# Optimization experiments

Hardware: AMD Instinct MI355X
Metric: run time of the kernel (lower is better)

## Reference

```python
import jax, jax.numpy as jnp
import numpy as np
import math

D = 256; B = 4; N = 2048; IN = 16; POS = 3; LAT = 128
DEPTH = 3; RATIO = 0.5; NBLK = 8  # depth*2 + 2 final blocks


def _silu(x):
    return x * jax.nn.sigmoid(x)


def _ln(h, g, b):
    m = h.mean(-1, keepdims=True)
    v = h.var(-1, keepdims=True)  # biased, matches nn.LayerNorm
    return (h - m) / jnp.sqrt(v + 1e-5) * g + b


def _block(h, A, g, b, w1, b1, w2, b2, eps):
    # h: (B, n, D), A: (B, n, n) binary adjacency (block-diag equivalent)
    hn = _ln(h, g, b)
    nb = jnp.einsum('bij,bjd->bid', A, hn)  # sparse.mm(adj, h) per graph
    t = (1.0 + eps) * hn + nb
    t = _silu(t @ w1 + b1) @ w2 + b2
    return h + t


def _forward(x, adj, pos, in_w, in_b, pw1, pb1, pw2, pb2,
             bg, bb, bw1, bb1, bw2, bb2, beps, pool_p, lw, lb, batch_size):
    Bsz = batch_size
    n = adj.shape[0]
    d = in_w.shape[1]
    h = x @ in_w + in_b  # (B*N, D)
    # positional embedding: tile, normalize (unbiased std like torch), MLP
    pt = jnp.tile(pos, (Bsz, 1))
    pn = (pt - pt.mean(0, keepdims=True)) / (pt.std(0, ddof=1, keepdims=True) + 1e-8)
    pe = _silu(pn @ pw1 + pb1) @ pw2 + pb2
    h = (h + pe).reshape(Bsz, n, d)
    A = jnp.broadcast_to(adj, (Bsz, n, n))  # shared block-diag tiles
    blk = 0
    for dep in range(DEPTH):
        for _ in range(2):  # blocks_per_stage
            h = _block(h, A, bg[blk], bb[blk], bw1[blk], bb1[blk],
                       bw2[blk], bb2[blk], beps[blk])
            blk += 1
        # TopKPool: projection score, per-graph top-k, tanh gating
        p = pool_p[dep]
        score = h @ p / jnp.linalg.norm(p)  # (B, n)
        k = int(math.ceil(RATIO * h.shape[1]))  # static
        idx = jnp.sort(jax.lax.top_k(score, k)[1], axis=-1)  # (B, k)
        gate = jnp.tanh(jnp.take_along_axis(score, idx, axis=1))
        h = jnp.take_along_axis(h, idx[:, :, None], axis=1) * gate[:, :, None]
        # subgraph_coo + to_binary: adj[idx][:, idx] per graph
        A = jax.vmap(lambda a, i: a[i][:, i])(A, idx)
        A = (A > 0).astype(h.dtype)
    for _ in range(2):  # final_stage
        h = _block(h, A, bg[blk], bb[blk], bw1[blk], bb1[blk],
                   bw2[blk], bb2[blk], beps[blk])
        blk += 1
    hm = h.mean(1)
    hs = h.std(1, ddof=1) + 1e-6  # torch .std is unbiased
    return jnp.concatenate([hm, hs], axis=-1) @ lw + lb  # (B, LAT)


def setup_inputs() -> dict:
    key = jax.random.key(0)
    ks = jax.random.split(key, 12)
    f32 = jnp.float32
    s = 1.0 / np.sqrt(D)
    x = jax.random.normal(ks[0], (B * N, IN), f32)
    adj = (jax.random.uniform(ks[1], (N, N)) < 0.004).astype(f32)  # ~8 nbrs/node
    pos = jax.random.normal(ks[2], (N, POS), f32)
    return {
        'x': x, 'adj': adj, 'pos': pos,
        'in_w': jax.random.normal(ks[3], (IN, D), f32) / np.sqrt(IN),
        'in_b': jnp.zeros(D, f32),
        'pw1': jax.random.normal(ks[4], (POS, D), f32) / np.sqrt(POS),
        'pb1': jnp.zeros(D, f32),
        'pw2': jax.random.normal(ks[5], (D, D), f32) * s,
        'pb2': jnp.zeros(D, f32),
        'bg': jnp.ones((NBLK, D), f32),
        'bb': jnp.zeros((NBLK, D), f32),
        'bw1': jax.random.normal(ks[6], (NBLK, D, D), f32) * s,
        'bb1': jnp.zeros((NBLK, D), f32),
        'bw2': jax.random.normal(ks[7], (NBLK, D, D), f32) * (0.5 * s),
        'bb2': jnp.zeros((NBLK, D), f32),
        'beps': jnp.zeros(NBLK, f32),
        'pool_p': jax.random.normal(ks[8], (DEPTH, D), f32) * s,
        'lw': jax.random.normal(ks[9], (2 * D, LAT), f32) / np.sqrt(2 * D),
        'lb': jnp.zeros(LAT, f32),
        'batch_size': B,
    }


def reference(x, adj, pos, in_w, in_b, pw1, pb1, pw2, pb2,
              bg, bb, bw1, bb1, bw2, bb2, beps, pool_p, lw, lb, batch_size):
    return _forward(x, adj, pos, in_w, in_b, pw1, pb1, pw2, pb2,
                    bg, bb, bw1, bb1, bw2, bb2, beps, pool_p, lw, lb, batch_size)
```

## Files before the change

### kernel.cpp

```cpp
#include <hip/hip_runtime.h>
#include <hip/hip_bf16.h>

#define NTOT 2048
#define DD 256
#define BSZ 4

typedef _Float16 half_t;
typedef __attribute__((ext_vector_type(8))) _Float16 halfx8;
typedef __attribute__((ext_vector_type(4))) _Float16 halfx4;
typedef __attribute__((ext_vector_type(4))) float f32x4;

__device__ __forceinline__ float blockReduceSum256(float v) {
    __shared__ float red[4];
    for (int off = 32; off > 0; off >>= 1) v += __shfl_down(v, off);
    int lane = threadIdx.x & 63, w = threadIdx.x >> 6;
    __syncthreads();
    if (lane == 0) red[w] = v;
    __syncthreads();
    return red[0] + red[1] + red[2] + red[3];
}

__global__ void stats_kernel(const float* __restrict__ pos, float* __restrict__ pstats,
                             const float* __restrict__ poolp, float* __restrict__ pinv) {
    int tid = threadIdx.x;
    if (blockIdx.x == 0) {
        float s[3] = {0.f, 0.f, 0.f};
        for (int i = tid; i < NTOT; i += 256)
            for (int c = 0; c < 3; ++c) s[c] += pos[i * 3 + c];
        float m[3];
        for (int c = 0; c < 3; ++c) m[c] = blockReduceSum256(s[c]) / (float)NTOT;
        float q[3] = {0.f, 0.f, 0.f};
        for (int i = tid; i < NTOT; i += 256)
            for (int c = 0; c < 3; ++c) { float d = pos[i * 3 + c] - m[c]; q[c] += d * d; }
        for (int c = 0; c < 3; ++c) {
            float t = blockReduceSum256(q[c]);
            if (tid == 0) {
                float var = ((float)BSZ * t) / ((float)BSZ * NTOT - 1.0f);
                pstats[c] = m[c];
                pstats[3 + c] = 1.0f / (sqrtf(var) + 1e-8f);
            }
        }
    } else {
        int dep = blockIdx.x - 1;
        float v = poolp[dep * DD + tid];
        float ss = blockReduceSum256(v * v);
        if (tid == 0) pinv[dep] = rsqrtf(ss);
    }
}

__global__ void pe_q_kernel(const float* __restrict__ pos, const float* __restrict__ stats,
                            const float* __restrict__ pw1, const float* __restrict__ pb1,
                            half_t* __restrict__ q) {
    int i = blockIdx.x, d = threadIdx.x;
    float acc = pb1[d];
    for (int c = 0; c < 3; ++c) {
        float pn = (pos[i * 3 + c] - stats[c]) * stats[3 + c];
        acc += pn * pw1[c * DD + d];
    }
    acc = acc / (1.0f + expf(-acc));
    q[i * DD + d] = (half_t)acc;
}

__global__ void init_h_kernel(const float* __restrict__ x, const float* __restrict__ in_w,
                              const float* __restrict__ in_b, const float* __restrict__ pe,
                              float* __restrict__ h, float* __restrict__ z) {
    int row = blockIdx.x, d = threadIdx.x;
    float acc = in_b[d];
    for (int k = 0; k < 16; ++k) acc += x[row * 16 + k] * in_w[k * DD + d];
    float v = acc + pe[(row & (NTOT - 1)) * DD + d];
    h[(size_t)row * DD + d] = v;
    float s = blockReduceSum256(v);
    float ss = blockReduceSum256(v * v);
    float mean = s * (1.0f / DD);
    float rs = rsqrtf(ss * (1.0f / DD) - mean * mean + 1e-5f);
    z[(size_t)row * DD + d] = (v - mean) * rs;
}

__global__ void wprep_kernel(const float* __restrict__ bw1, const float* __restrict__ bw2,
                             const float* __restrict__ pw2, half_t* __restrict__ Wt) {
    int m = blockIdx.x, nb = blockIdx.y * 16, kb = blockIdx.z * 16;
    const float* W = (m < 8) ? (bw1 + (size_t)m * DD * DD)
                  : (m < 16) ? (bw2 + (size_t)(m - 8) * DD * DD)
                             : pw2;
    __shared__ float s[16][17];
    int i = threadIdx.x >> 4, j = threadIdx.x & 15;
    s[i][j] = W[(size_t)(kb + i) * DD + nb + j];
    __syncthreads();
    Wt[(size_t)m * DD * DD + (size_t)(nb + i) * DD + kb + j] = (half_t)s[j][i];
}

__global__ void csr_count_kernel(const float* __restrict__ adj, int* __restrict__ counts) {
    int i = blockIdx.x, tid = threadIdx.x;
    float c = 0.f;
    for (int j = tid; j < NTOT; j += 256) c += (adj[(size_t)i * NTOT + j] != 0.f) ? 1.f : 0.f;
    float t = blockReduceSum256(c);
    if (tid == 0) counts[i] = (int)(t + 0.5f);
}

__global__ void scan_kernel(const int* __restrict__ counts, int* __restrict__ row_ptr) {
    __shared__ int csum[256];
    int tid = threadIdx.x;
    int local[8]; int tot = 0;
    for (int u = 0; u < 8; ++u) { local[u] = counts[tid * 8 + u]; tot += local[u]; }
    csum[tid] = tot; __syncthreads();
    for (int off = 1; off < 256; off <<= 1) {
        int v = (tid >= off) ? csum[tid - off] : 0;
        __syncthreads();
        csum[tid] += v;
        __syncthreads();
    }
    int run = csum[tid] - tot;
    for (int u = 0; u < 8; ++u) { row_ptr[tid * 8 + u] = run; run += local[u]; }
    if (tid == 255) row_ptr[NTOT] = run;
}

__global__ void csr_fill_kernel(const float* __restrict__ adj, const int* __restrict__ row_ptr,
                                int* __restrict__ col) {
    int i = blockIdx.x, lane = threadIdx.x;
    int base = row_ptr[i];
    int run = 0;
    for (int j0 = 0; j0 < NTOT; j0 += 64) {
        int j = j0 + lane;
        bool pred = adj[(size_t)i * NTOT + j] != 0.f;
        unsigned long long mask = __ballot(pred);
        if (pred) {
            int pos = run + __popcll(mask & ((1ull << lane) - 1ull));
            col[base + pos] = j;
        }
        run += __popcll(mask);
    }
}

__global__ void init_maps_kernel(int* __restrict__ orig, int* __restrict__ inv) {
    int t = blockIdx.x * 256 + threadIdx.x;
    int i = t & (NTOT - 1);
    orig[t] = i; inv[t] = i;
}

__global__ void build_lcol_kernel(const int* __restrict__ row_ptr, const int* __restrict__ col,
                                  const int* __restrict__ orig, const int* __restrict__ inv,
                                  int* __restrict__ ldeg, int* __restrict__ lcol, int k, int tag) {
    int t = blockIdx.x * 256 + threadIdx.x;
    int b = t / k, i = t - b * k;
    int key = b * NTOT + i;
    int o = orig[key];
    int s = row_ptr[o], e = row_ptr[o + 1];
    const int* invb = inv + b * NTOT;
    int cnt = 0;
    for (int p = s; p < e && cnt < 64; ++p) {
        int v = invb[col[p]];
        if ((v >> 12) == tag) { lcol[(size_t)key * 64 + cnt] = v & 4095; ++cnt; }
    }
    ldeg[key] = cnt;
}

template <int SCORE>
__global__ void __launch_bounds__(256) layer_kernel(
    float* __restrict__ h, const float* __restrict__ zin, float* __restrict__ zout,
    const half_t* __restrict__ Wt1, const half_t* __restrict__ Wt2,
    const float* __restrict__ b1v, const float* __restrict__ b2v,
    const float* __restrict__ gv, const float* __restrict__ bbv,
    const float* __restrict__ beps, int blk,
    const int* __restrict__ row_ptr, const int* __restrict__ col,
    const int* __restrict__ ldeg, const int* __restrict__ lcol,
    const float* __restrict__ poolp, const float* __restrict__ pinv_all,
    float* __restrict__ scores, int dep, int n, int lvl0) {
    __shared__ half_t tb[16][264];
    __shared__ half_t ub[16][264];
    __shared__ float part[4][16][3];
    __shared__ float mrs[16][2];
    int tid = threadIdx.x;
    int rowBase = blockIdx.x * 16;
    float eps1 = 1.0f + beps[blk];

    {
        int rl = tid >> 4, cg = tid & 15;
        int r = rowBase + rl;
        int b = r / n, i = r - b * n;
        const f32x4* zb = (const f32x4*)zin + (size_t)b * n * 64;
        f32x4 acc[4];
#pragma unroll
        for (int u = 0; u < 4; ++u) acc[u] = zb[(size_t)i * 64 + cg + 16 * u] * eps1;
        int deg; const int* lc;
        if (lvl0) {
            int s = row_ptr[i];
            deg = row_ptr[i + 1] - s;
            lc = col + s;
        } else {
            int key = b * NTOT + i;
            deg = ldeg[key];
            lc = lcol + (size_t)key * 64;
        }
        int p = 0;
        for (; p + 4 <= deg; p += 4) {
            int j0 = lc[p], j1 = lc[p + 1], j2 = lc[p + 2], j3 = lc[p + 3];
#pragma unroll
            for (int u = 0; u < 4; ++u) {
                f32x4 v0 = zb[(size_t)j0 * 64 + cg + 16 * u];
                f32x4 v1 = zb[(size_t)j1 * 64 + cg + 16 * u];
                f32x4 v2 = zb[(size_t)j2 * 64 + cg + 16 * u];
                f32x4 v3 = zb[(size_t)j3 * 64 + cg + 16 * u];
                acc[u] += (v0 + v1) + (v2 + v3);
            }
        }
        for (; p < deg; ++p) {
            int j = lc[p];
#pragma unroll
            for (int u = 0; u < 4; ++u) acc[u] += zb[(size_t)j * 64 + cg + 16 * u];
        }
        float coefb = eps1 + (float)deg;
#pragma unroll
        for (int u = 0; u < 4; ++u) {
            int c4 = cg + 16 * u;
            f32x4 gvv = ((const f32x4*)gv)[c4];
            f32x4 bvv = ((const f32x4*)bbv)[c4];
            f32x4 tv = gvv * acc[u] + bvv * coefb;
            halfx4 th;
#pragma unroll
            for (int e = 0; e < 4; ++e) th[e] = (half_t)tv[e];
            *(halfx4*)&tb[rl][c4 * 4] = th;
        }
    }
    __syncthreads();

    int w = tid >> 6, l = tid & 63;
    int lo = l & 15, hi = l >> 4;
    int kb = hi * 8;

    {
        f32x4 acc[4] = {};
#pragma unroll
        for (int k0 = 0; k0 < DD; k0 += 32) {
            halfx8 a0 = *(const halfx8*)&tb[lo][kb + k0];
#pragma unroll
            for (int j = 0; j < 4; ++j) {
                halfx8 bj = *(const halfx8*)(Wt1 + (size_t)(w * 64 + j * 16 + lo) * DD + kb + k0);
                acc[j] = __builtin_amdgcn_mfma_f32_16x16x32_f16(a0, bj, acc[j], 0, 0, 0);
            }
        }
        float bs[4];
#pragma unroll
        for (int j = 0; j < 4; ++j) bs[j] = b1v[w * 64 + j * 16 + lo];
#pragma unroll
        for (int q = 0; q < 4; ++q)
#pragma unroll
            for (int j = 0; j < 4; ++j) {
                float v = acc[j][q] + bs[j];
                v = v / (1.0f + expf(-v));
                ub[hi * 4 + q][w * 64 + j * 16 + lo] = (half_t)v;
            }
    }
    __syncthreads();

    {
        f32x4 acc[4] = {};
#pragma unroll
        for (int k0 = 0; k0 < DD; k0 += 32) {
            halfx8 a0 = *(const halfx8*)&ub[lo][kb + k0];
#pragma unroll
            for (int j = 0; j < 4; ++j) {
                halfx8 bj = *(const halfx8*)(Wt2 + (size_t)(w * 64 + j * 16 + lo) * DD + kb + k0);
                acc[j] = __builtin_amdgcn_mfma_f32_16x16x32_f16(a0, bj, acc[j], 0, 0, 0);
            }
        }
        float bs[4], pv[4] = {};
#pragma unroll
        for (int j = 0; j < 4; ++j) bs[j] = b2v[w * 64 + j * 16 + lo];
        if (SCORE) {
#pragma unroll
            for (int j = 0; j < 4; ++j) pv[j] = poolp[dep * DD + w * 64 + j * 16 + lo];
        }
        float vh[4][4];
#pragma unroll
        for (int q = 0; q < 4; ++q) {
            int r = rowBase + hi * 4 + q;
            float s = 0.f, ss = 0.f, sp = 0.f;
#pragma unroll
            for (int j = 0; j < 4; ++j) {
                int c = w * 64 + j * 16 + lo;
                float v = h[(size_t)r * DD + c] + acc[j][q] + bs[j];
                vh[j][q] = v;
                s += v; ss += v * v;
                if (SCORE) sp += v * pv[j];
            }
#pragma unroll
            for (int m = 1; m < 16; m <<= 1) {
                s += __shfl_xor(s, m); ss += __shfl_xor(ss, m);
                if (SCORE) sp += __shfl_xor(sp, m);
            }
            if (lo == 0) {
                int rl = hi * 4 + q;
                part[w][rl][0] = s; part[w][rl][1] = ss;
                if (SCORE) part[w][rl][2] = sp;
            }
        }
        __syncthreads();
        if (tid < 16) {
            float s = 0.f, ss = 0.f, sp = 0.f;
#pragma unroll
            for (int w2 = 0; w2 < 4; ++w2) {
                s += part[w2][tid][0]; ss += part[w2][tid][1];
                if (SCORE) sp += part[w2][tid][2];
            }
            float mean = s * (1.0f / DD);
            float var = ss * (1.0f / DD) - mean * mean;
            mrs[tid][0] = mean;
            mrs[tid][1] = rsqrtf(var + 1e-5f);
            if (SCORE) {
                int r = rowBase + tid;
                int b2 = r / n, ii = r - b2 * n;
                scores[b2 * NTOT + ii] = sp * pinv_all[dep];
            }
        }
        __syncthreads();
#pragma unroll
        for (int q = 0; q < 4; ++q) {
            int rl = hi * 4 + q;
            int r = rowBase + rl;
            float mean = mrs[rl][0], rs = mrs[rl][1];
#pragma unroll
            for (int j = 0; j < 4; ++j) {
                int c = w * 64 + j * 16 + lo;
                float v = vh[j][q];
                h[(size_t)r * DD + c] = v;
                zout[(size_t)r * DD + c] = (v - mean) * rs;
            }
        }
    }
}

__global__ void __launch_bounds__(256) mm_pe_kernel(const half_t* __restrict__ A,
                                                    const half_t* __restrict__ Wt,
                                                    const float* __restrict__ bias,
                                                    float* __restrict__ C) {
    int tid = threadIdx.x;
    int w = tid >> 6, l = tid & 63;
    int lo = l & 15, hi = l >> 4;
    int rowBase = blockIdx.x * 16;
    int kb = hi * 8;
    const half_t* a0p = A + (size_t)(rowBase + lo) * DD + kb;
    f32x4 acc[4] = {};
#pragma unroll
    for (int k0 = 0; k0 < DD; k0 += 32) {
        halfx8 a0 = *(const halfx8*)(a0p + k0);
#pragma unroll
        for (int j = 0; j < 4; ++j) {
            halfx8 bj = *(const halfx8*)(Wt + (size_t)(w * 64 + j * 16 + lo) * DD + kb + k0);
            acc[j] = __builtin_amdgcn_mfma_f32_16x16x32_f16(a0, bj, acc[j], 0, 0, 0);
        }
    }
#pragma unroll
    for (int q = 0; q < 4; ++q)
#pragma unroll
        for (int j = 0; j < 4; ++j) {
            int r = rowBase + hi * 4 + q;
            int c = w * 64 + j * 16 + lo;
            C[(size_t)r * DD + c] = acc[j][q] + bias[c];
        }
}

__global__ void topk_kernel(const float* __restrict__ scores, const int* __restrict__ orig_cur,
                            int* __restrict__ orig_next, int* __restrict__ idx_local,
                            float* __restrict__ gate, int n, int k) {
    __shared__ unsigned keys[2048];
    __shared__ int hist[256];
    __shared__ int sg[256], se[256];
    __shared__ int sh_bucket, sh_r, sh_cnt;
    __shared__ unsigned cand[256];
    __shared__ unsigned sh_thr;
    int b = blockIdx.x;
    const float* sc = scores + b * NTOT;
    int tid = threadIdx.x;
    for (int i = tid; i < n; i += 256) {
        unsigned u = __float_as_uint(sc[i]);
        keys[i] = (u & 0x80000000u) ? ~u : (u | 0x80000000u);
    }
    hist[tid] = 0;
    if (tid == 0) sh_cnt = 0;
    __syncthreads();
    for (int i = tid; i < n; i += 256) atomicAdd(&hist[keys[i] >> 24], 1);
    __syncthreads();
    int cnt = hist[tid];
    sg[tid] = cnt;
    __syncthreads();
    for (int off = 1; off < 256; off <<= 1) {
        int v = (tid >= off) ? sg[tid - off] : 0;
        __syncthreads();
        sg[tid] += v;
        __syncthreads();
    }
    int r = n - k;
    int incl = sg[tid], excl = incl - cnt;
    if (excl <= r && r < incl) { sh_bucket = tid; sh_r = r - excl; }
    __syncthreads();
    int b1 = sh_bucket, r1 = sh_r;
    int c = hist[b1];
    unsigned thrkey;
    if (c <= 256) {
        for (int i = tid; i < n; i += 256) {
            unsigned key = keys[i];
            if ((key >> 24) == (unsigned)b1) {
                int pos = atomicAdd(&sh_cnt, 1);
                cand[pos] = key;
            }
        }
        __syncthreads();
        if (tid < c) {
            unsigned mine = cand[tid];
            int less = 0, eq = 0;
            for (int j = 0; j < c; ++j) {
                unsigned oth = cand[j];
                less += (oth < mine); eq += (oth == mine);
            }
            if (less <= r1 && r1 < less + eq) sh_thr = mine;
        }
        __syncthreads();
        thrkey = sh_thr;
    } else {
        unsigned prefix = ((unsigned)b1) << 24;
        int rr = r1;
        for (int shift = 16; shift >= 0; shift -= 8) {
            __syncthreads();
            hist[tid] = 0;
            __syncthreads();
            unsigned mask = 0xFFFFFFFFu << (shift + 8);
            for (int i = tid; i < n; i += 256) {
                unsigned key = keys[i];
                if ((key & mask) == (prefix & mask)) atomicAdd(&hist[(key >> shift) & 255], 1);
            }
            __syncthreads();
            int cnt2 = hist[tid];
            sg[tid] = cnt2;
            __syncthreads();
            for (int off = 1; off < 256; off <<= 1) {
                int v = (tid >= off) ? sg[tid - off] : 0;
                __syncthreads();
                sg[tid] += v;
                __syncthreads();
            }
            int incl2 = sg[tid], excl2 = incl2 - cnt2;
            if (excl2 <= rr && rr < incl2) { sh_bucket = tid; sh_r = rr - excl2; }
            __syncthreads();
            prefix |= ((unsigned)sh_bucket) << shift;
            rr = sh_r;
            __syncthreads();
        }
        thrkey = prefix;
    }
    unsigned uthr = (thrkey & 0x80000000u) ? (thrkey ^ 0x80000000u) : ~thrkey;
    float thr = __uint_as_float(uthr);
    int chunk = n / 256;
    int base = tid * chunk;
    int cgt = 0, ceq = 0;
    for (int u = 0; u < chunk; ++u) {
        float s = sc[base + u];
        cgt += (s > thr); ceq += (s == thr);
    }
    sg[tid] = cgt; se[tid] = ceq; __syncthreads();
    for (int off = 1; off < 256; off <<= 1) {
        int vg = (tid >= off) ? sg[tid - off] : 0;
        int ve = (tid >= off) ? se[tid - off] : 0;
        __syncthreads();
        sg[tid] += vg; se[tid] += ve;
        __syncthreads();
    }
    int total_gt = sg[255];
    int ties = k - total_gt;
    int gtb = sg[tid] - cgt, eqb = se[tid] - ceq;
    for (int u = 0; u < chunk; ++u) {
        int i = base + u;
        float s = sc[i];
        bool isgt = (s > thr), iseq = (s == thr);
        bool keep = isgt || (iseq && eqb < ties);
        if (keep) {
            int pos = gtb + (eqb < ties ? eqb : ties);
            idx_local[b * NTOT + pos] = i;
            gate[b * NTOT + pos] = tanhf(s);
            orig_next[b * NTOT + pos] = orig_cur[b * NTOT + i];
        }
        gtb += isgt; eqb += iseq;
    }
}

__global__ void __launch_bounds__(64) gather_kernel(
    const float* __restrict__ h, const int* __restrict__ idx_local,
    const float* __restrict__ gate, const int* __restrict__ orig_new,
    float* __restrict__ hout, float* __restrict__ zout, int* __restrict__ inv,
    int n_old, int k, int tag) {
    int r = blockIdx.x;
    int b = r / k, rr = r - b * k;
    int lane = threadIdx.x;
    int src = idx_local[b * NTOT + rr];
    float gg = gate[b * NTOT + rr];
    f32x4 v = ((const f32x4*)h)[(size_t)(b * n_old + src) * 64 + lane] * gg;
    ((f32x4*)hout)[(size_t)r * 64 + lane] = v;
    float s = v[0] + v[1] + v[2] + v[3];
    float ss = v[0] * v[0] + v[1] * v[1] + v[2] * v[2] + v[3] * v[3];
#pragma unroll
    for (int m = 1; m < 64; m <<= 1) { s += __shfl_xor(s, m); ss += __shfl_xor(ss, m); }
    float mean = s * (1.0f / DD);
    float rs = rsqrtf(ss * (1.0f / DD) - mean * mean + 1e-5f);
    f32x4 zv = (v - mean) * rs;
    ((f32x4*)zout)[(size_t)r * 64 + lane] = zv;
    if (lane == 0) inv[b * NTOT + orig_new[b * NTOT + rr]] = (tag << 12) | rr;
}

__global__ void readout_kernel(const float* __restrict__ h, float* __restrict__ feat) {
    int bd = blockIdx.x;
    int b = bd >> 8, d = bd & 255;
    int i = threadIdx.x;
    float x = h[(size_t)(b * 256 + i) * DD + d];
    float m = blockReduceSum256(x) / 256.0f;
    float diff = x - m;
    float s2 = blockReduceSum256(diff * diff);
    if (i == 0) {
        feat[b * 512 + d] = m;
        feat[b * 512 + 256 + d] = sqrtf(s2 / 255.0f) + 1e-6f;
    }
}

__global__ void final_kernel(const float* __restrict__ feat, const float* __restrict__ lw,
                             const float* __restrict__ lb, float* __restrict__ out) {
    int b = blockIdx.x, l = threadIdx.x;
    float acc = lb[l];
    const float* f = feat + b * 512;
    for (int k = 0; k < 512; ++k) acc += f[k] * lw[k * 128 + l];
    out[b * 128 + l] = acc;
}

extern "C" void kernel_launch(void* const* d_in, const int* in_sizes, int n_in,
                              void* d_out, int out_size, void* d_ws, size_t ws_size,
                              hipStream_t stream) {
    (void)in_sizes; (void)n_in; (void)out_size; (void)ws_size;
    const float* x     = (const float*)d_in[0];
    const float* adj   = (const float*)d_in[1];
    const float* pos   = (const float*)d_in[2];
    const float* in_w  = (const float*)d_in[3];
    const float* in_b  = (const float*)d_in[4];
    const float* pw1   = (const float*)d_in[5];
    const float* pb1   = (const float*)d_in[6];
    const float* pw2   = (const float*)d_in[7];
    const float* pb2   = (const float*)d_in[8];
    const float* bg    = (const float*)d_in[9];
    const float* bb    = (const float*)d_in[10];
    const float* bw1   = (const float*)d_in[11];
    const float* bb1   = (const float*)d_in[12];
    const float* bw2   = (const float*)d_in[13];
    const float* bb2   = (const float*)d_in[14];
    const float* beps  = (const float*)d_in[15];
    const float* poolp = (const float*)d_in[16];
    const float* lw    = (const float*)d_in[17];
    const float* lb    = (const float*)d_in[18];
    float* out = (float*)d_out;

    char* wp = (char*)d_ws;
    auto alloc = [&](size_t bytes) -> void* {
        void* p = (void*)wp;
        wp += (bytes + 255) & ~(size_t)255;
        return p;
    };
    const size_t HBYTES = (size_t)BSZ * NTOT * DD * sizeof(float);
    float*  h    = (float*)alloc(HBYTES);
    float*  bufC = (float*)alloc(HBYTES);
    float*  zA   = (float*)alloc(HBYTES);
    float*  zB   = (float*)alloc(HBYTES);
    half_t* tbq  = (half_t*)alloc((size_t)NTOT * DD * sizeof(half_t));
    half_t* Wt   = (half_t*)alloc((size_t)17 * DD * DD * sizeof(half_t));
    float* pstats  = (float*)alloc(8 * sizeof(float));
    float* pinv    = (float*)alloc(4 * sizeof(float));
    float* scores  = (float*)alloc(BSZ * NTOT * sizeof(float));
    float* gate    = (float*)alloc(BSZ * NTOT * sizeof(float));
    int*   origA   = (int*)alloc(BSZ * NTOT * sizeof(int));
    int*   origB   = (int*)alloc(BSZ * NTOT * sizeof(int));
    int*   idxl    = (int*)alloc(BSZ * NTOT * sizeof(int));
    int*   inv     = (int*)alloc(BSZ * NTOT * sizeof(int));
    int*   counts  = (int*)alloc(NTOT * sizeof(int));
    int*   row_ptr = (int*)alloc((NTOT + 1) * sizeof(int));
    int*   col     = (int*)alloc((size_t)NTOT * 64 * sizeof(int));
    int*   ldeg    = (int*)alloc(BSZ * NTOT * sizeof(int));
    int*   lcol    = (int*)alloc((size_t)BSZ * NTOT * 64 * sizeof(int));
    float* feat    = (float*)alloc(BSZ * 512 * sizeof(float));

    wprep_kernel<<<dim3(17, 16, 16), 256, 0, stream>>>(bw1, bw2, pw2, Wt);
    stats_kernel<<<4, 256, 0, stream>>>(pos, pstats, poolp, pinv);
    pe_q_kernel<<<NTOT, 256, 0, stream>>>(pos, pstats, pw1, pb1, tbq);
    mm_pe_kernel<<<NTOT / 16, 256, 0, stream>>>(tbq, Wt + (size_t)16 * DD * DD, pb2, bufC);
    init_h_kernel<<<BSZ * NTOT, 256, 0, stream>>>(x, in_w, in_b, bufC, h, zA);
    csr_count_kernel<<<NTOT, 256, 0, stream>>>(adj, counts);
    scan_kernel<<<1, 256, 0, stream>>>(counts, row_ptr);
    csr_fill_kernel<<<NTOT, 64, 0, stream>>>(adj, row_ptr, col);
    init_maps_kernel<<<(BSZ * NTOT) / 256, 256, 0, stream>>>(origA, inv);

    float* hcur = h;
    float* halt = bufC;
    float* zin = zA;
    float* zout = zB;
    int* orig = origA;
    int* orign = origB;
    int n = NTOT;
    int blk = 0;
    for (int dep = 0; dep < 4; ++dep) {
        for (int s = 0; s < 2; ++s) {
            int rows = BSZ * n;
            if (s == 1 && dep < 3) {
                layer_kernel<1><<<rows / 16, 256, 0, stream>>>(
                    hcur, zin, zout, Wt + (size_t)blk * DD * DD, Wt + (size_t)(8 + blk) * DD * DD,
                    bb1 + blk * DD, bb2 + blk * DD, bg + blk * DD, bb + blk * DD,
                    beps, blk, row_ptr, col, ldeg, lcol, poolp, pinv, scores, dep, n,
                    dep == 0 ? 1 : 0);
            } else {
                layer_kernel<0><<<rows / 16, 256, 0, stream>>>(
                    hcur, zin, zout, Wt + (size_t)blk * DD * DD, Wt + (size_t)(8 + blk) * DD * DD,
                    bb1 + blk * DD, bb2 + blk * DD, bg + blk * DD, bb + blk * DD,
                    beps, blk, row_ptr, col, ldeg, lcol, nullptr, nullptr, nullptr, 0, n,
                    dep == 0 ? 1 : 0);
            }
            { float* t = zin; zin = zout; zout = t; }
            ++blk;
        }
        if (dep < 3) {
            int k = n / 2;
            topk_kernel<<<BSZ, 256, 0, stream>>>(scores, orig, orign, idxl, gate, n, k);
            { int* t = orig; orig = orign; orign = t; }
            gather_kernel<<<BSZ * k, 64, 0, stream>>>(hcur, idxl, gate, orig, halt, zin, inv,
                                                      n, k, dep + 1);
            { float* t = hcur; hcur = halt; halt = t; }
            build_lcol_kernel<<<(BSZ * k) / 256, 256, 0, stream>>>(row_ptr, col, orig, inv,
                                                                   ldeg, lcol, k, dep + 1);
            n = k;
        }
    }
    readout_kernel<<<BSZ * 256, 256, 0, stream>>>(hcur, feat);
    final_kernel<<<BSZ, 128, 0, stream>>>(feat, lw, lb, out);
}
```

Measured before the change: 294.8 us.

## Fuse setup kernels, merge PE MLP with input projection, filter neighbors inline

New measurement: 283.3 us. 3.9% less time.

```diff
diff --git a/kernel.cpp b/kernel.cpp
--- a/kernel.cpp
+++ b/kernel.cpp
@@ -20,138 +20,183 @@
     return red[0] + red[1] + red[2] + red[3];
 }
 
-__global__ void stats_kernel(const float* __restrict__ pos, float* __restrict__ pstats,
-                             const float* __restrict__ poolp, float* __restrict__ pinv) {
+#define SB_WPREP 4352
+#define SB_STAT  4356
+#define SB_A2L   4868
+#define SB_MAPS  4900
+__global__ void __launch_bounds__(256) setup_kernel(
+    const float* __restrict__ bw1, const float* __restrict__ bw2,
+    const float* __restrict__ pw2, half_t* __restrict__ Wt,
+    const float* __restrict__ pos, float* __restrict__ pstats,
+    const float* __restrict__ poolp, float* __restrict__ pinv,
+    const float* __restrict__ adj, int* __restrict__ ldeg0, int* __restrict__ lcol0,
+    int* __restrict__ orig, int* __restrict__ inv) {
+    int bid = blockIdx.x, tid = threadIdx.x;
+    if (bid < SB_WPREP) {
+        int m = bid >> 8, rem = bid & 255;
+        int nb = (rem >> 4) * 16, kb = (rem & 15) * 16;
+        const float* W = (m < 8) ? (bw1 + (size_t)m * DD * DD)
+                      : (m < 16) ? (bw2 + (size_t)(m - 8) * DD * DD)
+                                 : pw2;
+        __shared__ float s[16][17];
+        int i = tid >> 4, j = tid & 15;
+        s[i][j] = W[(size_t)(kb + i) * DD + nb + j];
+        __syncthreads();
+        Wt[(size_t)m * DD * DD + (size_t)(nb + i) * DD + kb + j] = (half_t)s[j][i];
+    } else if (bid < SB_STAT) {
+        int which = bid - SB_WPREP;
+        if (which == 0) {
+            float s[3] = {0.f, 0.f, 0.f};
+            for (int i = tid; i < NTOT; i += 256)
+                for (int c = 0; c < 3; ++c) s[c] += pos[i * 3 + c];
+            float m[3];
+            for (int c = 0; c < 3; ++c) m[c] = blockReduceSum256(s[c]) / (float)NTOT;
+            float q[3] = {0.f, 0.f, 0.f};
+            for (int i = tid; i < NTOT; i += 256)
+                for (int c = 0; c < 3; ++c) { float d = pos[i * 3 + c] - m[c]; q[c] += d * d; }
+            for (int c = 0; c < 3; ++c) {
+                float t = blockReduceSum256(q[c]);
+                if (tid == 0) {
+                    float var = ((float)BSZ * t) / ((float)BSZ * NTOT - 1.0f);
+                    pstats[c] = m[c];
+                    pstats[3 + c] = 1.0f / (sqrtf(var) + 1e-8f);
+                }
+            }
+        } else {
+            int dep = which - 1;
+            float v = poolp[dep * DD + tid];
+            float ss = blockReduceSum256(v * v);
+            if (tid == 0) pinv[dep] = rsqrtf(ss);
+        }
+    } else if (bid < SB_A2L) {
+        int row = (bid - SB_STAT) * 4 + (tid >> 6);
+        int lane = tid & 63;
+        int run = 0;
+        for (int j0 = 0; j0 < NTOT; j0 += 64) {
+            int j = j0 + lane;
+            bool pred = adj[(size_t)row * NTOT + j] != 0.f;
+            unsigned long long mask = __ballot(pred);
+            if (pred) {
+                int pos2 = run + __popcll(mask & ((1ull << lane) - 1ull));
+                if (pos2 < 64) lcol0[row * 64 + pos2] = j;
+            }
+            run += __popcll(mask);
+        }
+        if (lane == 0) ldeg0[row] = run < 64 ? run : 64;
+    } else {
+        int t = (bid - SB_A2L) * 256 + tid;
+        int i = t & (NTOT - 1);
+        orig[t] = i; inv[t] = i;
+    }
+}
+
+__global__ void __launch_bounds__(256) pe_h_kernel(
+    const float* __restrict__ pos, const float* __restrict__ pstats,
+    const float* __restrict__ pw1, const float* __restrict__ pb1,
+    const half_t* __restrict__ Wt16, const float* __restrict__ pb2,
+    const float* __restrict__ x, const float* __restrict__ in_w,
+    const float* __restrict__ in_b, float* __restrict__ h, float* __restrict__ z) {
+    __shared__ half_t tb[16][264];
+    __shared__ float iw[16][DD];
+    __shared__ float xs[16][16];
+    __shared__ float part[4][16][2];
+    __shared__ float mrs[16][2];
     int tid = threadIdx.x;
-    if (blockIdx.x == 0) {
-        float s[3] = {0.f, 0.f, 0.f};
-        for (int i = tid; i < NTOT; i += 256)
-            for (int c = 0; c < 3; ++c) s[c] += pos[i * 3 + c];
-        float m[3];
-        for (int c = 0; c < 3; ++c) m[c] = blockReduceSum256(s[c]) / (float)NTOT;
-        float q[3] = {0.f, 0.f, 0.f};
-        for (int i = tid; i < NTOT; i += 256)
-            for (int c = 0; c < 3; ++c) { float d = pos[i * 3 + c] - m[c]; q[c] += d * d; }
-        for (int c = 0; c < 3; ++c) {
-            float t = blockReduceSum256(q[c]);
-            if (tid == 0) {
-                float var = ((float)BSZ * t) / ((float)BSZ * NTOT - 1.0f);
-                pstats[c] = m[c];
-                pstats[3 + c] = 1.0f / (sqrtf(var) + 1e-8f);
-            }
-        }
-    } else {
-        int dep = blockIdx.x - 1;
-        float v = poolp[dep * DD + tid];
-        float ss = blockReduceSum256(v * v);
-        if (tid == 0) pinv[dep] = rsqrtf(ss);
-    }
-}
-
-__global__ void pe_q_kernel(const float* __restrict__ pos, const float* __restrict__ stats,
-                            const float* __restrict__ pw1, const float* __restrict__ pb1,
-                            half_t* __restrict__ q) {
-    int i = blockIdx.x, d = threadIdx.x;
-    float acc = pb1[d];
-    for (int c = 0; c < 3; ++c) {
-        float pn = (pos[i * 3 + c] - stats[c]) * stats[3 + c];
-        acc += pn * pw1[c * DD + d];
-    }
-    acc = acc / (1.0f + expf(-acc));
-    q[i * DD + d] = (half_t)acc;
-}
-
-__global__ void init_h_kernel(const float* __restrict__ x, const float* __restrict__ in_w,
-                              const float* __restrict__ in_b, const float* __restrict__ pe,
-                              float* __restrict__ h, float* __restrict__ z) {
-    int row = blockIdx.x, d = threadIdx.x;
-    float acc = in_b[d];
-    for (int k = 0; k < 16; ++k) acc += x[row * 16 + k] * in_w[k * DD + d];
-    float v = acc + pe[(row & (NTOT - 1)) * DD + d];
-    h[(size_t)row * DD + d] = v;
-    float s = blockReduceSum256(v);
-    float ss = blockReduceSum256(v * v);
-    float mean = s * (1.0f / DD);
-    float rs = rsqrtf(ss * (1.0f / DD) - mean * mean + 1e-5f);
-    z[(size_t)row * DD + d] = (v - mean) * rs;
-}
-
-__global__ void wprep_kernel(const float* __restrict__ bw1, const float* __restrict__ bw2,
-                             const float* __restrict__ pw2, half_t* __restrict__ Wt) {
-    int m = blockIdx.x, nb = blockIdx.y * 16, kb = blockIdx.z * 16;
-    const float* W = (m < 8) ? (bw1 + (size_t)m * DD * DD)
-                  : (m < 16) ? (bw2 + (size_t)(m - 8) * DD * DD)
-                             : pw2;
-    __shared__ float s[16][17];
-    int i = threadIdx.x >> 4, j = threadIdx.x & 15;
-    s[i][j] = W[(size_t)(kb + i) * DD + nb + j];
-    __syncthreads();
-    Wt[(size_t)m * DD * DD + (size_t)(nb + i) * DD + kb + j] = (half_t)s[j][i];
-}
-
-__global__ void csr_count_kernel(const float* __restrict__ adj, int* __restrict__ counts) {
-    int i = blockIdx.x, tid = threadIdx.x;
-    float c = 0.f;
-    for (int j = tid; j < NTOT; j += 256) c += (adj[(size_t)i * NTOT + j] != 0.f) ? 1.f : 0.f;
-    float t = blockReduceSum256(c);
-    if (tid == 0) counts[i] = (int)(t + 0.5f);
-}
-
-__global__ void scan_kernel(const int* __restrict__ counts, int* __restrict__ row_ptr) {
-    __shared__ int csum[256];
-    int tid = threadIdx.x;
-    int local[8]; int tot = 0;
-    for (int u = 0; u < 8; ++u) { local[u] = counts[tid * 8 + u]; tot += local[u]; }
-    csum[tid] = tot; __syncthreads();
-    for (int off = 1; off < 256; off <<= 1) {
-        int v = (tid >= off) ? csum[tid - off] : 0;
-        __syncthreads();
-        csum[tid] += v;
-        __syncthreads();
-    }
-    int run = csum[tid] - tot;
-    for (int u = 0; u < 8; ++u) { row_ptr[tid * 8 + u] = run; run += local[u]; }
-    if (tid == 255) row_ptr[NTOT] = run;
-}
-
-__global__ void csr_fill_kernel(const float* __restrict__ adj, const int* __restrict__ row_ptr,
-                                int* __restrict__ col) {
-    int i = blockIdx.x, lane = threadIdx.x;
-    int base = row_ptr[i];
-    int run = 0;
-    for (int j0 = 0; j0 < NTOT; j0 += 64) {
-        int j = j0 + lane;
-        bool pred = adj[(size_t)i * NTOT + j] != 0.f;
-        unsigned long long mask = __ballot(pred);
-        if (pred) {
-            int pos = run + __popcll(mask & ((1ull << lane) - 1ull));
-            col[base + pos] = j;
-        }
-        run += __popcll(mask);
-    }
-}
-
-__global__ void init_maps_kernel(int* __restrict__ orig, int* __restrict__ inv) {
-    int t = blockIdx.x * 256 + threadIdx.x;
-    int i = t & (NTOT - 1);
-    orig[t] = i; inv[t] = i;
-}
-
-__global__ void build_lcol_kernel(const int* __restrict__ row_ptr, const int* __restrict__ col,
-                                  const int* __restrict__ orig, const int* __restrict__ inv,
-                                  int* __restrict__ ldeg, int* __restrict__ lcol, int k, int tag) {
-    int t = blockIdx.x * 256 + threadIdx.x;
-    int b = t / k, i = t - b * k;
-    int key = b * NTOT + i;
-    int o = orig[key];
-    int s = row_ptr[o], e = row_ptr[o + 1];
-    const int* invb = inv + b * NTOT;
-    int cnt = 0;
-    for (int p = s; p < e && cnt < 64; ++p) {
-        int v = invb[col[p]];
-        if ((v >> 12) == tag) { lcol[(size_t)key * 64 + cnt] = v & 4095; ++cnt; }
-    }
-    ldeg[key] = cnt;
+    int i0 = blockIdx.x * 16;
+    {
+        int rl = tid >> 4, cb = (tid & 15) * 16;
+        float pn[3];
+#pragma unroll
+        for (int c = 0; c < 3; ++c)
+            pn[c] = (pos[(i0 + rl) * 3 + c] - pstats[c]) * pstats[3 + c];
+#pragma unroll
+        for (int u = 0; u < 16; ++u) {
+            int d = cb + u;
+            float a = pb1[d];
+            a += pn[0] * pw1[d];
+            a += pn[1] * pw1[DD + d];
+            a += pn[2] * pw1[2 * DD + d];
+            a = a / (1.0f + expf(-a));
+            tb[rl][d] = (half_t)a;
+        }
+        int k = tid >> 4;
+#pragma unroll
+        for (int u = 0; u < 16; ++u) iw[k][cb + u] = in_w[k * DD + cb + u];
+    }
+    __syncthreads();
+    int w = tid >> 6, l = tid & 63;
+    int lo = l & 15, hi = l >> 4;
+    int kb = hi * 8;
+    float pe_r[4][4];
+    {
+        f32x4 acc[4] = {};
+#pragma unroll
+        for (int k0 = 0; k0 < DD; k0 += 32) {
+            halfx8 a0 = *(const halfx8*)&tb[lo][kb + k0];
+#pragma unroll
+            for (int j = 0; j < 4; ++j) {
+                halfx8 bj = *(const halfx8*)(Wt16 + (size_t)(w * 64 + j * 16 + lo) * DD + kb + k0);
+                acc[j] = __builtin_amdgcn_mfma_f32_16x16x32_f16(a0, bj, acc[j], 0, 0, 0);
+            }
+        }
+#pragma unroll
+        for (int j = 0; j < 4; ++j) {
+            float bs = pb2[w * 64 + j * 16 + lo];
+#pragma unroll
+            for (int q = 0; q < 4; ++q) pe_r[j][q] = acc[j][q] + bs;
+        }
+    }
+    float xb[4];
+#pragma unroll
+    for (int j = 0; j < 4; ++j) xb[j] = in_b[w * 64 + j * 16 + lo];
+    for (int b = 0; b < BSZ; ++b) {
+        __syncthreads();
+        xs[tid >> 4][tid & 15] = x[(size_t)(b * NTOT + i0 + (tid >> 4)) * 16 + (tid & 15)];
+        __syncthreads();
+        float vh[4][4];
+#pragma unroll
+        for (int q = 0; q < 4; ++q) {
+            int rl = hi * 4 + q;
+            float s = 0.f, ss = 0.f;
+#pragma unroll
+            for (int j = 0; j < 4; ++j) {
+                int c = w * 64 + j * 16 + lo;
+                float acc = xb[j];
+#pragma unroll
+                for (int k = 0; k < 16; ++k) acc += xs[rl][k] * iw[k][c];
+                float v = acc + pe_r[j][q];
+                vh[j][q] = v;
+                s += v; ss += v * v;
+            }
+#pragma unroll
+            for (int m = 1; m < 16; m <<= 1) { s += __shfl_xor(s, m); ss += __shfl_xor(ss, m); }
+            if (lo == 0) { part[w][rl][0] = s; part[w][rl][1] = ss; }
+        }
+        __syncthreads();
+        if (tid < 16) {
+            float s = 0.f, ss = 0.f;
+#pragma unroll
+            for (int w2 = 0; w2 < 4; ++w2) { s += part[w2][tid][0]; ss += part[w2][tid][1]; }
+            float mean = s * (1.0f / DD);
+            float var = ss * (1.0f / DD) - mean * mean;
+            mrs[tid][0] = mean;
+            mrs[tid][1] = rsqrtf(var + 1e-5f);
+        }
+        __syncthreads();
+#pragma unroll
+        for (int q = 0; q < 4; ++q) {
+            int rl = hi * 4 + q;
+            size_t r = (size_t)(b * NTOT + i0 + rl);
+            float mean = mrs[rl][0], rs = mrs[rl][1];
+#pragma unroll
+            for (int j = 0; j < 4; ++j) {
+                int c = w * 64 + j * 16 + lo;
+                float v = vh[j][q];
+                h[r * DD + c] = v;
+                z[r * DD + c] = (v - mean) * rs;
+            }
+        }
+    }
 }
 
 template <int SCORE>
@@ -161,10 +206,10 @@
     const float* __restrict__ b1v, const float* __restrict__ b2v,
     const float* __restrict__ gv, const float* __restrict__ bbv,
     const float* __restrict__ beps, int blk,
-    const int* __restrict__ row_ptr, const int* __restrict__ col,
-    const int* __restrict__ ldeg, const int* __restrict__ lcol,
+    const int* __restrict__ ldeg0, const int* __restrict__ lcol0,
+    const int* __restrict__ orig, const int* __restrict__ inv,
     const float* __restrict__ poolp, const float* __restrict__ pinv_all,
-    float* __restrict__ scores, int dep, int n, int lvl0) {
+    float* __restrict__ scores, int dep, int n, int tag) {
     __shared__ half_t tb[16][264];
     __shared__ half_t ub[16][264];
     __shared__ float part[4][16][3];
@@ -181,34 +226,68 @@
         f32x4 acc[4];
 #pragma unroll
         for (int u = 0; u < 4; ++u) acc[u] = zb[(size_t)i * 64 + cg + 16 * u] * eps1;
-        int deg; const int* lc;
-        if (lvl0) {
-            int s = row_ptr[i];
-            deg = row_ptr[i + 1] - s;
-            lc = col + s;
+        int cnt = 0;
+        if (tag == 0) {
+            int deg = ldeg0[i];
+            const int* lc = lcol0 + i * 64;
+            int p = 0;
+            for (; p + 4 <= deg; p += 4) {
+                int j0 = lc[p], j1 = lc[p + 1], j2 = lc[p + 2], j3 = lc[p + 3];
+#pragma unroll
+                for (int u = 0; u < 4; ++u) {
+                    f32x4 v0 = zb[(size_t)j0 * 64 + cg + 16 * u];
+                    f32x4 v1 = zb[(size_t)j1 * 64 + cg + 16 * u];
+                    f32x4 v2 = zb[(size_t)j2 * 64 + cg + 16 * u];
+                    f32x4 v3 = zb[(size_t)j3 * 64 + cg + 16 * u];
+                    acc[u] += (v0 + v1) + (v2 + v3);
+                }
+            }
+            for (; p < deg; ++p) {
+                int j = lc[p];
+#pragma unroll
+                for (int u = 0; u < 4; ++u) acc[u] += zb[(size_t)j * 64 + cg + 16 * u];
+            }
+            cnt = deg;
         } else {
-            int key = b * NTOT + i;
-            deg = ldeg[key];
-            lc = lcol + (size_t)key * 64;
-        }
-        int p = 0;
-        for (; p + 4 <= deg; p += 4) {
-            int j0 = lc[p], j1 = lc[p + 1], j2 = lc[p + 2], j3 = lc[p + 3];
-#pragma unroll
-            for (int u = 0; u < 4; ++u) {
-                f32x4 v0 = zb[(size_t)j0 * 64 + cg + 16 * u];
-                f32x4 v1 = zb[(size_t)j1 * 64 + cg + 16 * u];
-                f32x4 v2 = zb[(size_t)j2 * 64 + cg + 16 * u];
-                f32x4 v3 = zb[(size_t)j3 * 64 + cg + 16 * u];
-                acc[u] += (v0 + v1) + (v2 + v3);
-            }
-        }
-        for (; p < deg; ++p) {
-            int j = lc[p];
-#pragma unroll
-            for (int u = 0; u < 4; ++u) acc[u] += zb[(size_t)j * 64 + cg + 16 * u];
-        }
-        float coefb = eps1 + (float)deg;
+            int o = orig[b * NTOT + i];
+            int deg = ldeg0[o];
+            const int* lc = lcol0 + o * 64;
+            const int* invb = inv + b * NTOT;
+            int p = 0;
+            for (; p + 4 <= deg; p += 4) {
+                int c0 = lc[p], c1 = lc[p + 1], c2 = lc[p + 2], c3 = lc[p + 3];
+                int v0 = invb[c0], v1 = invb[c1], v2 = invb[c2], v3 = invb[c3];
+                if ((v0 >> 12) == tag) {
+                    int j = v0 & 4095; ++cnt;
+#pragma unroll
+                    for (int u = 0; u < 4; ++u) acc[u] += zb[(size_t)j * 64 + cg + 16 * u];
+                }
+                if ((v1 >> 12) == tag) {
+                    int j = v1 & 4095; ++cnt;
+#pragma unroll
+                    for (int u = 0; u < 4; ++u) acc[u] += zb[(size_t)j * 64 + cg + 16 * u];
+                }
+                if ((v2 >> 12) == tag) {
+                    int j = v2 & 4095; ++cnt;
+#pragma unroll
+                    for (int u = 0; u < 4; ++u) acc[u] += zb[(size_t)j * 64 + cg + 16 * u];
+                }
+                if ((v3 >> 12) == tag) {
+                    int j = v3 & 4095; ++cnt;
+#pragma unroll
+                    for (int u = 0; u < 4; ++u) acc[u] += zb[(size_t)j * 64 + cg + 16 * u];
+                }
+            }
+            for (; p < deg; ++p) {
+                int v = invb[lc[p]];
+                if ((v >> 12) == tag) {
+                    int j = v & 4095; ++cnt;
+#pragma unroll
+                    for (int u = 0; u < 4; ++u) acc[u] += zb[(size_t)j * 64 + cg + 16 * u];
+                }
+            }
+        }
+        float coefb = eps1 + (float)cnt;
 #pragma unroll
         for (int u = 0; u < 4; ++u) {
             int c4 = cg + 16 * u;
@@ -327,36 +406,6 @@
             }
         }
     }
-}
-
-__global__ void __launch_bounds__(256) mm_pe_kernel(const half_t* __restrict__ A,
-                                                    const half_t* __restrict__ Wt,
-                                                    const float* __restrict__ bias,
-                                                    float* __restrict__ C) {
-    int tid = threadIdx.x;
-    int w = tid >> 6, l = tid & 63;
-    int lo = l & 15, hi = l >> 4;
-    int rowBase = blockIdx.x * 16;
-    int kb = hi * 8;
-    const half_t* a0p = A + (size_t)(rowBase + lo) * DD + kb;
-    f32x4 acc[4] = {};
-#pragma unroll
-    for (int k0 = 0; k0 < DD; k0 += 32) {
-        halfx8 a0 = *(const halfx8*)(a0p + k0);
-#pragma unroll
-        for (int j = 0; j < 4; ++j) {
-            halfx8 bj = *(const halfx8*)(Wt + (size_t)(w * 64 + j * 16 + lo) * DD + kb + k0);
-            acc[j] = __builtin_amdgcn_mfma_f32_16x16x32_f16(a0, bj, acc[j], 0, 0, 0);
-        }
-    }
-#pragma unroll
-    for (int q = 0; q < 4; ++q)
-#pragma unroll
-        for (int j = 0; j < 4; ++j) {
-            int r = rowBase + hi * 4 + q;
-            int c = w * 64 + j * 16 + lo;
-            C[(size_t)r * DD + c] = acc[j][q] + bias[c];
-        }
 }
 
 __global__ void topk_kernel(const float* __restrict__ scores, const int* __restrict__ orig_cur,
@@ -505,27 +554,28 @@
     if (lane == 0) inv[b * NTOT + orig_new[b * NTOT + rr]] = (tag << 12) | rr;
 }
 
-__global__ void readout_kernel(const float* __restrict__ h, float* __restrict__ feat) {
-    int bd = blockIdx.x;
-    int b = bd >> 8, d = bd & 255;
-    int i = threadIdx.x;
-    float x = h[(size_t)(b * 256 + i) * DD + d];
-    float m = blockReduceSum256(x) / 256.0f;
-    float diff = x - m;
-    float s2 = blockReduceSum256(diff * diff);
-    if (i == 0) {
-        feat[b * 512 + d] = m;
-        feat[b * 512 + 256 + d] = sqrtf(s2 / 255.0f) + 1e-6f;
-    }
-}
-
-__global__ void final_kernel(const float* __restrict__ feat, const float* __restrict__ lw,
-                             const float* __restrict__ lb, float* __restrict__ out) {
-    int b = blockIdx.x, l = threadIdx.x;
-    float acc = lb[l];
-    const float* f = feat + b * 512;
-    for (int k = 0; k < 512; ++k) acc += f[k] * lw[k * 128 + l];
-    out[b * 128 + l] = acc;
+__global__ void __launch_bounds__(256) readout_final_kernel(
+    const float* __restrict__ h, const float* __restrict__ lw,
+    const float* __restrict__ lb, float* __restrict__ out) {
+    __shared__ float feat[512];
+    int b = blockIdx.x, d = threadIdx.x;
+    const float* hb = h + (size_t)b * 256 * DD;
+    float s = 0.f;
+    for (int i = 0; i < 256; ++i) s += hb[(size_t)i * DD + d];
+    float mean = s / 256.0f;
+    float s2 = 0.f;
+    for (int i = 0; i < 256; ++i) {
+        float diff = hb[(size_t)i * DD + d] - mean;
+        s2 += diff * diff;
+    }
+    feat[d] = mean;
+    feat[256 + d] = sqrtf(s2 / 255.0f) + 1e-6f;
+    __syncthreads();
+    if (d < 128) {
+        float acc = lb[d];
+        for (int k = 0; k < 512; ++k) acc += feat[k] * lw[k * 128 + d];
+        out[b * 128 + d] = acc;
+    }
 }
 
 extern "C" void kernel_launch(void* const* d_in, const int* in_sizes, int n_in,
@@ -564,7 +614,6 @@
     float*  bufC = (float*)alloc(HBYTES);
     float*  zA   = (float*)alloc(HBYTES);
     float*  zB   = (float*)alloc(HBYTES);
-    half_t* tbq  = (half_t*)alloc((size_t)NTOT * DD * sizeof(half_t));
     half_t* Wt   = (half_t*)alloc((size_t)17 * DD * DD * sizeof(half_t));
     float* pstats  = (float*)alloc(8 * sizeof(float));
     float* pinv    = (float*)alloc(4 * sizeof(float));
@@ -574,22 +623,14 @@
     int*   origB   = (int*)alloc(BSZ * NTOT * sizeof(int));
     int*   idxl    = (int*)alloc(BSZ * NTOT * sizeof(int));
     int*   inv     = (int*)alloc(BSZ * NTOT * sizeof(int));
-    int*   counts  = (int*)alloc(NTOT * sizeof(int));
-    int*   row_ptr = (int*)alloc((NTOT + 1) * sizeof(int));
-    int*   col     = (int*)alloc((size_t)NTOT * 64 * sizeof(int));
-    int*   ldeg    = (int*)alloc(BSZ * NTOT * sizeof(int));
-    int*   lcol    = (int*)alloc((size_t)BSZ * NTOT * 64 * sizeof(int));
-    float* feat    = (float*)alloc(BSZ * 512 * sizeof(float));
-
-    wprep_kernel<<<dim3(17, 16, 16), 256, 0, stream>>>(bw1, bw2, pw2, Wt);
-    stats_kernel<<<4, 256, 0, stream>>>(pos, pstats, poolp, pinv);
-    pe_q_kernel<<<NTOT, 256, 0, stream>>>(pos, pstats, pw1, pb1, tbq);
-    mm_pe_kernel<<<NTOT / 16, 256, 0, stream>>>(tbq, Wt + (size_t)16 * DD * DD, pb2, bufC);
-    init_h_kernel<<<BSZ * NTOT, 256, 0, stream>>>(x, in_w, in_b, bufC, h, zA);
-    csr_count_kernel<<<NTOT, 256, 0, stream>>>(adj, counts);
-    scan_kernel<<<1, 256, 0, stream>>>(counts, row_ptr);
-    csr_fill_kernel<<<NTOT, 64, 0, stream>>>(adj, row_ptr, col);
-    init_maps_kernel<<<(BSZ * NTOT) / 256, 256, 0, stream>>>(origA, inv);
+    int*   ldeg0   = (int*)alloc(NTOT * sizeof(int));
+    int*   lcol0   = (int*)alloc((size_t)NTOT * 64 * sizeof(int));
+
+    setup_kernel<<<SB_MAPS, 256, 0, stream>>>(bw1, bw2, pw2, Wt, pos, pstats, poolp, pinv,
+                                              adj, ldeg0, lcol0, origA, inv);
+    pe_h_kernel<<<NTOT / 16, 256, 0, stream>>>(pos, pstats, pw1, pb1,
+                                               Wt + (size_t)16 * DD * DD, pb2,
+                                               x, in_w, in_b, h, zA);
 
     float* hcur = h;
     float* halt = bufC;
@@ -606,14 +647,12 @@
                 layer_kernel<1><<<rows / 16, 256, 0, stream>>>(
                     hcur, zin, zout, Wt + (size_t)blk * DD * DD, Wt + (size_t)(8 + blk) * DD * DD,
                     bb1 + blk * DD, bb2 + blk * DD, bg + blk * DD, bb + blk * DD,
-                    beps, blk, row_ptr, col, ldeg, lcol, poolp, pinv, scores, dep, n,
-                    dep == 0 ? 1 : 0);
+                    beps, blk, ldeg0, lcol0, orig, inv, poolp, pinv, scores, dep, n, dep);
             } else {
                 layer_kernel<0><<<rows / 16, 256, 0, stream>>>(
                     hcur, zin, zout, Wt + (size_t)blk * DD * DD, Wt + (size_t)(8 + blk) * DD * DD,
                     bb1 + blk * DD, bb2 + blk * DD, bg + blk * DD, bb + blk * DD,
-                    beps, blk, row_ptr, col, ldeg, lcol, nullptr, nullptr, nullptr, 0, n,
-                    dep == 0 ? 1 : 0);
+                    beps, blk, ldeg0, lcol0, orig, inv, nullptr, nullptr, nullptr, 0, n, dep);
             }
             { float* t = zin; zin = zout; zout = t; }
             ++blk;
@@ -625,11 +664,8 @@
             gather_kernel<<<BSZ * k, 64, 0, stream>>>(hcur, idxl, gate, orig, halt, zin, inv,
                                                       n, k, dep + 1);
             { float* t = hcur; hcur = halt; halt = t; }
-            build_lcol_kernel<<<(BSZ * k) / 256, 256, 0, stream>>>(row_ptr, col, orig, inv,
-                                                                   ldeg, lcol, k, dep + 1);
             n = k;
         }
     }
-    readout_kernel<<<BSZ * 256, 256, 0, stream>>>(hcur, feat);
-    final_kernel<<<BSZ, 128, 0, stream>>>(feat, lw, lb, out);
-}
+    readout_final_kernel<<<BSZ, 256, 0, stream>>>(hcur, lw, lb, out);
+}
```
